# Kernel tuning notes

Hardware: AMD Instinct MI355X
Metric: run time of the kernel (lower is better)

The kernel has to match this reference:

```python
import jax, jax.numpy as jnp
import numpy as np

N = 50000       # nodes
E = 800000      # edges (before self-loops)
F_IN = 128      # per-head input features (nfeat * t_size, t_size=1)
NHID = 128
NHEADS = 4
NCLASS = 64
NEG_SLOPE = 0.2   # GATConv leakyrelu negative_slope
ALPHA = 0.2       # outer LeakyReLU(alpha)


def setup_inputs():
    key = jax.random.key(0)
    ks = jax.random.split(key, 10)
    type_emb = jax.random.normal(ks[0], (NHEADS, N, F_IN), jnp.float32)
    edge = jax.random.randint(ks[1], (2, E), 0, N, dtype=jnp.int32)
    W = jax.random.normal(ks[2], (NHEADS, F_IN, NHID), jnp.float32) / np.sqrt(F_IN).astype(np.float32)
    att_src = jax.random.normal(ks[3], (NHEADS, NHID), jnp.float32) * 0.1
    att_dst = jax.random.normal(ks[4], (NHEADS, NHID), jnp.float32) * 0.1
    bias = jnp.zeros((NHEADS, NHID), jnp.float32)
    W_out = jax.random.normal(ks[5], (NHID * NHEADS, NCLASS), jnp.float32) / np.sqrt(NHID * NHEADS).astype(np.float32)
    att_src_out = jax.random.normal(ks[6], (NCLASS,), jnp.float32) * 0.1
    att_dst_out = jax.random.normal(ks[7], (NCLASS,), jnp.float32) * 0.1
    bias_out = jnp.zeros((NCLASS,), jnp.float32)
    return {"type_emb": type_emb, "edge": edge, "W": W, "att_src": att_src,
            "att_dst": att_dst, "bias": bias, "W_out": W_out,
            "att_src_out": att_src_out, "att_dst_out": att_dst_out,
            "bias_out": bias_out}


def _gat_conv(x, src, dst, W, a_src, a_dst, b):
    """PyG GATConv, heads=1, with self-loops already in (src, dst)."""
    xs = x @ W                                      # [N, H]
    e = jax.nn.leaky_relu((xs @ a_src)[src] + (xs @ a_dst)[dst], NEG_SLOPE)  # [E']
    # segment softmax over destination nodes (every node has a self-loop -> no empty segment)
    m = jax.ops.segment_max(e, dst, num_segments=N)
    ex = jnp.exp(e - m[dst])
    denom = jax.ops.segment_sum(ex, dst, num_segments=N)
    alpha = ex / denom[dst]                          # [E']
    out = jax.ops.segment_sum(alpha[:, None] * xs[src], dst, num_segments=N)  # [N, H]
    return out + b


def reference(type_emb, edge, W, att_src, att_dst, bias, W_out,
              att_src_out, att_dst_out, bias_out):
    loop = jnp.arange(N, dtype=edge.dtype)
    src = jnp.concatenate([edge[0], loop])
    dst = jnp.concatenate([edge[1], loop])
    # per-head GraphAttentionLayer: GATConv -> LeakyReLU(alpha) (dropout inactive)
    heads = [jax.nn.leaky_relu(
                 _gat_conv(type_emb[i], src, dst, W[i], att_src[i], att_dst[i], bias[i]),
                 ALPHA)
             for i in range(NHEADS)]
    x = jnp.concatenate(heads, axis=1)               # [N, NHID*NHEADS]
    y = jax.nn.leaky_relu(
            _gat_conv(x, src, dst, W_out, att_src_out, att_dst_out, bias_out),
            ALPHA)
    return jnp.tanh(y)                               # [N, NCLASS]
```

## Files before the change

kernel.cpp:

```cpp
#include <hip/hip_runtime.h>
#include <cmath>

#define NN 50000
#define EE 800000
#define ETOT (EE + NN)
#define NSCAN ((NN + 1023) / 1024)
#define SROWS 50048

typedef __bf16 v8bf __attribute__((ext_vector_type(8)));
typedef float f32x4 __attribute__((ext_vector_type(4)));

__device__ __forceinline__ float lrelu(float x){ return x > 0.0f ? x : 0.2f * x; }
__device__ __forceinline__ unsigned short f2bf_rne(float x){
  unsigned int u = __float_as_uint(x);
  u += 0x7fffu + ((u >> 16) & 1u);
  return (unsigned short)(u >> 16);
}
__device__ __forceinline__ float bf2f(unsigned short b){
  return __uint_as_float(((unsigned int)b) << 16);
}
__device__ __forceinline__ void fma8(float* acc, float w, uint4 u){
  acc[0] += w * __uint_as_float(u.x << 16);
  acc[1] += w * __uint_as_float(u.x & 0xffff0000u);
  acc[2] += w * __uint_as_float(u.y << 16);
  acc[3] += w * __uint_as_float(u.y & 0xffff0000u);
  acc[4] += w * __uint_as_float(u.z << 16);
  acc[5] += w * __uint_as_float(u.z & 0xffff0000u);
  acc[6] += w * __uint_as_float(u.w << 16);
  acc[7] += w * __uint_as_float(u.w & 0xffff0000u);
}

__global__ void k_hist(const int* __restrict__ dst, int* __restrict__ cnt){
  int i = blockIdx.x * 256 + threadIdx.x;
  if (i >= ETOT) return;
  int d = (i < EE) ? dst[i] : (i - EE);
  atomicAdd(&cnt[d], 1);
}

__global__ void k_scan1(const int* __restrict__ cnt, int* __restrict__ part){
  __shared__ int sm[256];
  int b = blockIdx.x, t = threadIdx.x;
  int base = b * 1024 + t * 4;
  int s = 0;
  #pragma unroll
  for (int j = 0; j < 4; j++) if (base + j < NN) s += cnt[base + j];
  sm[t] = s; __syncthreads();
  for (int off = 128; off; off >>= 1){
    if (t < off) sm[t] += sm[t + off];
    __syncthreads();
  }
  if (t == 0) part[b] = sm[0];
}

__global__ void k_scan2(const int* __restrict__ part, int* __restrict__ part2){
  if (threadIdx.x == 0 && blockIdx.x == 0){
    int run = 0;
    for (int i = 0; i < NSCAN; i++){ part2[i] = run; run += part[i]; }
  }
}

__global__ void k_scan3(const int* __restrict__ cnt, const int* __restrict__ part2,
                        int* __restrict__ rowptr){
  __shared__ int sm[256];
  int b = blockIdx.x, t = threadIdx.x;
  int base = b * 1024 + t * 4;
  int v[4]; int s = 0;
  #pragma unroll
  for (int j = 0; j < 4; j++){ v[j] = (base + j < NN) ? cnt[base + j] : 0; s += v[j]; }
  sm[t] = s; __syncthreads();
  for (int off = 1; off < 256; off <<= 1){
    int x = (t >= off) ? sm[t - off] : 0;
    __syncthreads();
    sm[t] += x;
    __syncthreads();
  }
  int run = part2[b] + sm[t] - s;
  #pragma unroll
  for (int j = 0; j < 4; j++){
    if (base + j < NN){ rowptr[base + j] = run; run += v[j]; }
  }
  if (b == 0 && t == 0) rowptr[NN] = ETOT;
}

__global__ void k_scatter(const int* __restrict__ src, const int* __restrict__ dst,
                          const int* __restrict__ rowptr, int* __restrict__ fill,
                          int* __restrict__ csr){
  int i = blockIdx.x * 256 + threadIdx.x;
  if (i >= ETOT) return;
  int s, d;
  if (i < EE){ s = src[i]; d = dst[i]; } else { s = d = i - EE; }
  int pos = rowptr[d] + atomicAdd(&fill[d], 1);
  csr[pos] = s;
}

__global__ void k_convB(const float* __restrict__ B, unsigned short* __restrict__ bh,
                        unsigned short* __restrict__ bl, int K, int N, int total){
  int i = blockIdx.x * 256 + threadIdx.x;
  if (i >= total) return;
  int per = K * N;
  int h = i / per, rem = i - h * per;
  int k = rem / N, n = rem - k * N;
  float x = B[i];
  unsigned short hb = f2bf_rne(x);
  unsigned short lb = f2bf_rne(x - bf2f(hb));
  size_t o = (size_t)h * per + ((size_t)(k >> 3) * N + n) * 8 + (k & 7);
  bh[o] = hb; bl[o] = lb;
}

template<int BN, int OSTR>
__global__ __launch_bounds__(256) void gemm_split(const float* __restrict__ A,
                                                  const unsigned short* __restrict__ Bh,
                                                  const unsigned short* __restrict__ Bl,
                                                  unsigned short* __restrict__ out,
                                                  int M, int K,
                                                  const float* __restrict__ att_s,
                                                  const float* __restrict__ att_d,
                                                  float* __restrict__ ssrc,
                                                  float* __restrict__ sdst){
  const int t = threadIdx.x;
  const int wv = t >> 6, lane = t & 63;
  const int m0 = blockIdx.x * 128;
  const int h = blockIdx.y;
  A  += (size_t)h * M * K;
  Bh += (size_t)h * (K >> 3) * BN * 8;
  Bl += (size_t)h * (K >> 3) * BN * 8;
  const int colOff = h * BN;

  __shared__ v8bf sAh[4][128];
  __shared__ v8bf sAl[4][128];
  __shared__ v8bf sBh[4][BN];
  __shared__ v8bf sBl[4][BN];

  f32x4 acc[2][BN / 16];
  #pragma unroll
  for (int i = 0; i < 2; i++)
    #pragma unroll
    for (int j = 0; j < BN / 16; j++){
      f32x4 z = {0.f, 0.f, 0.f, 0.f};
      acc[i][j] = z;
    }

  const int mRow = t & 127;
  const int kh = (t >> 7) * 16;
  const bool valid = (m0 + mRow) < M;
  const int q = lane >> 4, lm = lane & 15;

  for (int k0 = 0; k0 < K; k0 += 32){
    const float* ap = A + (size_t)(m0 + mRow) * K + k0 + kh;
    float4 v0, v1, v2, v3;
    if (valid){
      v0 = *(const float4*)(ap);
      v1 = *(const float4*)(ap + 4);
      v2 = *(const float4*)(ap + 8);
      v3 = *(const float4*)(ap + 12);
    } else {
      v0 = v1 = v2 = v3 = make_float4(0.f, 0.f, 0.f, 0.f);
    }
    #pragma unroll
    for (int g = 0; g < 2; g++){
      float xv[8];
      if (g == 0){ xv[0]=v0.x; xv[1]=v0.y; xv[2]=v0.z; xv[3]=v0.w; xv[4]=v1.x; xv[5]=v1.y; xv[6]=v1.z; xv[7]=v1.w; }
      else       { xv[0]=v2.x; xv[1]=v2.y; xv[2]=v2.z; xv[3]=v2.w; xv[4]=v3.x; xv[5]=v3.y; xv[6]=v3.z; xv[7]=v3.w; }
      union { v8bf v; unsigned short u[8]; } H, L;
      #pragma unroll
      for (int i = 0; i < 8; i++){
        unsigned short hb = f2bf_rne(xv[i]);
        H.u[i] = hb;
        L.u[i] = f2bf_rne(xv[i] - bf2f(hb));
      }
      int k8 = (kh >> 3) + g;
      sAh[k8][mRow] = H.v;
      sAl[k8][mRow] = L.v;
    }
    {
      const v8bf* gh = (const v8bf*)Bh + (size_t)(k0 >> 3) * BN;
      const v8bf* gl = (const v8bf*)Bl + (size_t)(k0 >> 3) * BN;
      v8bf* dh = &sBh[0][0];
      v8bf* dl = &sBl[0][0];
      #pragma unroll
      for (int i = t; i < 4 * BN; i += 256){ dh[i] = gh[i]; dl[i] = gl[i]; }
    }
    __syncthreads();
    v8bf ah[2], al[2];
    #pragma unroll
    for (int rt = 0; rt < 2; rt++){
      int m = wv * 32 + rt * 16 + lm;
      ah[rt] = sAh[q][m];
      al[rt] = sAl[q][m];
    }
    #pragma unroll
    for (int ct = 0; ct < BN / 16; ct++){
      v8bf bh = sBh[q][ct * 16 + lm];
      v8bf bl = sBl[q][ct * 16 + lm];
      #pragma unroll
      for (int rt = 0; rt < 2; rt++){
        acc[rt][ct] = __builtin_amdgcn_mfma_f32_16x16x32_bf16(ah[rt], bh, acc[rt][ct], 0, 0, 0);
        acc[rt][ct] = __builtin_amdgcn_mfma_f32_16x16x32_bf16(ah[rt], bl, acc[rt][ct], 0, 0, 0);
        acc[rt][ct] = __builtin_amdgcn_mfma_f32_16x16x32_bf16(al[rt], bh, acc[rt][ct], 0, 0, 0);
      }
    }
    __syncthreads();
  }

  float asv[BN / 16], adv[BN / 16];
  #pragma unroll
  for (int ct = 0; ct < BN / 16; ct++){
    asv[ct] = att_s[h * BN + ct * 16 + lm];
    adv[ct] = att_d[h * BN + ct * 16 + lm];
  }

  #pragma unroll
  for (int rt = 0; rt < 2; rt++){
    #pragma unroll
    for (int reg = 0; reg < 4; reg++){
      int r = m0 + wv * 32 + rt * 16 + q * 4 + reg;
      float d0 = 0.f, d1 = 0.f;
      #pragma unroll
      for (int ct = 0; ct < BN / 16; ct++){
        float v = acc[rt][ct][reg];
        d0 += v * asv[ct];
        d1 += v * adv[ct];
      }
      #pragma unroll
      for (int off = 1; off < 16; off <<= 1){
        d0 += __shfl_xor(d0, off, 64);
        d1 += __shfl_xor(d1, off, 64);
      }
      if (r < M){
        unsigned short* orow = out + (size_t)r * OSTR + colOff + lm;
        #pragma unroll
        for (int ct = 0; ct < BN / 16; ct++)
          orow[ct * 16] = f2bf_rne(acc[rt][ct][reg]);
        if (lm == 0){
          ssrc[(size_t)h * SROWS + r] = d0;
          sdst[(size_t)h * SROWS + r] = d1;
        }
      }
    }
  }
}

template<int BN, int OSTR>
__global__ __launch_bounds__(256) void gemm_ps(const unsigned short* __restrict__ Ah,
                                               const unsigned short* __restrict__ Al,
                                               const unsigned short* __restrict__ Bh,
                                               const unsigned short* __restrict__ Bl,
                                               unsigned short* __restrict__ out,
                                               int M, int K,
                                               const float* __restrict__ att_s,
                                               const float* __restrict__ att_d,
                                               float* __restrict__ ssrc,
                                               float* __restrict__ sdst){
  const int t = threadIdx.x;
  const int wv = t >> 6, lane = t & 63;
  const int m0 = blockIdx.x * 128;
  const int h = blockIdx.y;
  const int colOff = h * BN;

  __shared__ v8bf sAh[4][128];
  __shared__ v8bf sAl[4][128];
  __shared__ v8bf sBh[4][BN];
  __shared__ v8bf sBl[4][BN];

  f32x4 acc[2][BN / 16];
  #pragma unroll
  for (int i = 0; i < 2; i++)
    #pragma unroll
    for (int j = 0; j < BN / 16; j++){
      f32x4 z = {0.f, 0.f, 0.f, 0.f};
      acc[i][j] = z;
    }

  const int mRow = t & 127;
  const int kh = (t >> 7) * 16;
  const bool valid = (m0 + mRow) < M;
  const int q = lane >> 4, lm = lane & 15;

  for (int k0 = 0; k0 < K; k0 += 32){
    const unsigned short* aph = Ah + (size_t)(m0 + mRow) * K + k0 + kh;
    const unsigned short* apl = Al + (size_t)(m0 + mRow) * K + k0 + kh;
    uint4 h0, h1, l0, l1;
    if (valid){
      h0 = *(const uint4*)(aph);
      h1 = *(const uint4*)(aph + 8);
      l0 = *(const uint4*)(apl);
      l1 = *(const uint4*)(apl + 8);
    } else {
      h0 = h1 = l0 = l1 = make_uint4(0, 0, 0, 0);
    }
    int k8 = kh >> 3;
    sAh[k8][mRow]     = *(v8bf*)&h0;
    sAh[k8 + 1][mRow] = *(v8bf*)&h1;
    sAl[k8][mRow]     = *(v8bf*)&l0;
    sAl[k8 + 1][mRow] = *(v8bf*)&l1;
    {
      const v8bf* gh = (const v8bf*)Bh + (size_t)(k0 >> 3) * BN;
      const v8bf* gl = (const v8bf*)Bl + (size_t)(k0 >> 3) * BN;
      v8bf* dh = &sBh[0][0];
      v8bf* dl = &sBl[0][0];
      #pragma unroll
      for (int i = t; i < 4 * BN; i += 256){ dh[i] = gh[i]; dl[i] = gl[i]; }
    }
    __syncthreads();
    v8bf ah[2], al[2];
    #pragma unroll
    for (int rt = 0; rt < 2; rt++){
      int m = wv * 32 + rt * 16 + lm;
      ah[rt] = sAh[q][m];
      al[rt] = sAl[q][m];
    }
    #pragma unroll
    for (int ct = 0; ct < BN / 16; ct++){
      v8bf bh = sBh[q][ct * 16 + lm];
      v8bf bl = sBl[q][ct * 16 + lm];
      #pragma unroll
      for (int rt = 0; rt < 2; rt++){
        acc[rt][ct] = __builtin_amdgcn_mfma_f32_16x16x32_bf16(ah[rt], bh, acc[rt][ct], 0, 0, 0);
        acc[rt][ct] = __builtin_amdgcn_mfma_f32_16x16x32_bf16(ah[rt], bl, acc[rt][ct], 0, 0, 0);
        acc[rt][ct] = __builtin_amdgcn_mfma_f32_16x16x32_bf16(al[rt], bh, acc[rt][ct], 0, 0, 0);
      }
    }
    __syncthreads();
  }

  float asv[BN / 16], adv[BN / 16];
  #pragma unroll
  for (int ct = 0; ct < BN / 16; ct++){
    asv[ct] = att_s[h * BN + ct * 16 + lm];
    adv[ct] = att_d[h * BN + ct * 16 + lm];
  }

  #pragma unroll
  for (int rt = 0; rt < 2; rt++){
    #pragma unroll
    for (int reg = 0; reg < 4; reg++){
      int r = m0 + wv * 32 + rt * 16 + q * 4 + reg;
      float d0 = 0.f, d1 = 0.f;
      #pragma unroll
      for (int ct = 0; ct < BN / 16; ct++){
        float v = acc[rt][ct][reg];
        d0 += v * asv[ct];
        d1 += v * adv[ct];
      }
      #pragma unroll
      for (int off = 1; off < 16; off <<= 1){
        d0 += __shfl_xor(d0, off, 64);
        d1 += __shfl_xor(d1, off, 64);
      }
      if (r < M){
        unsigned short* orow = out + (size_t)r * OSTR + colOff + lm;
        #pragma unroll
        for (int ct = 0; ct < BN / 16; ct++)
          orow[ct * 16] = f2bf_rne(acc[rt][ct][reg]);
        if (lm == 0){
          ssrc[(size_t)h * SROWS + r] = d0;
          sdst[(size_t)h * SROWS + r] = d1;
        }
      }
    }
  }
}

__global__ __launch_bounds__(256) void k_agg1(const int* __restrict__ rowptr,
                                              const int* __restrict__ csr,
                                              const float* __restrict__ ssrc,
                                              const float* __restrict__ sdst,
                                              const unsigned short* __restrict__ xs_all,
                                              const float* __restrict__ bias,
                                              unsigned short* __restrict__ x1h,
                                              unsigned short* __restrict__ x1l){
  int tid = blockIdx.x * 256 + threadIdx.x;
  int n = tid >> 4;
  int lm = threadIdx.x & 15;
  int h = blockIdx.y;
  if (n >= NN) return;
  int start = rowptr[n], end = rowptr[n + 1];
  const float* sp = ssrc + (size_t)h * SROWS;
  float sdn = sdst[(size_t)h * SROWS + n];
  const uint4* xp = (const uint4*)xs_all + h * 16 + lm;

  float sloc = 0.f;
  float acc[8];
  #pragma unroll
  for (int i = 0; i < 8; i++) acc[i] = 0.f;

  int e = start;
  int sA = csr[e];
  float svA = sp[sA];
  uint4 uA = xp[(size_t)sA * 64];
  for (; e + 1 < end; e++){
    int sB = csr[e + 1];
    float svB = sp[sB];
    uint4 uB = xp[(size_t)sB * 64];
    float w = __expf(lrelu(svA + sdn));
    sloc += w;
    fma8(acc, w, uA);
    svA = svB; uA = uB;
  }
  float w = __expf(lrelu(svA + sdn));
  sloc += w;
  fma8(acc, w, uA);

  float inv = 1.f / sloc;

  const float* bp = bias + h * 128 + lm * 8;
  float4 b0 = *(const float4*)bp, b1 = *(const float4*)(bp + 4);
  float bb[8] = {b0.x, b0.y, b0.z, b0.w, b1.x, b1.y, b1.z, b1.w};
  union { uint4 q; unsigned short u[8]; } HH, LL;
  #pragma unroll
  for (int i = 0; i < 8; i++){
    float o = lrelu(acc[i] * inv + bb[i]);
    unsigned short hb = f2bf_rne(o);
    HH.u[i] = hb;
    LL.u[i] = f2bf_rne(o - bf2f(hb));
  }
  size_t ofs = (size_t)n * 512 + h * 128 + lm * 8;
  *(uint4*)(x1h + ofs) = HH.q;
  *(uint4*)(x1l + ofs) = LL.q;
}

__global__ __launch_bounds__(256) void k_agg2(const int* __restrict__ rowptr,
                                              const int* __restrict__ csr,
                                              const float* __restrict__ ssrc,
                                              const float* __restrict__ sdst,
                                              const unsigned short* __restrict__ xs2,
                                              const float* __restrict__ bias,
                                              float* __restrict__ outp){
  int tid = blockIdx.x * 256 + threadIdx.x;
  int n = tid >> 3;
  int lm = threadIdx.x & 7;
  if (n >= NN) return;
  int start = rowptr[n], end = rowptr[n + 1];
  float sdn = sdst[n];
  const uint4* xp = (const uint4*)xs2 + lm;

  float sloc = 0.f;
  float acc[8];
  #pragma unroll
  for (int i = 0; i < 8; i++) acc[i] = 0.f;

  int e = start;
  int sA = csr[e];
  float svA = ssrc[sA];
  uint4 uA = xp[(size_t)sA * 8];
  for (; e + 1 < end; e++){
    int sB = csr[e + 1];
    float svB = ssrc[sB];
    uint4 uB = xp[(size_t)sB * 8];
    float w = __expf(lrelu(svA + sdn));
    sloc += w;
    fma8(acc, w, uA);
    svA = svB; uA = uB;
  }
  float w = __expf(lrelu(svA + sdn));
  sloc += w;
  fma8(acc, w, uA);

  float inv = 1.f / sloc;

  float o[8];
  #pragma unroll
  for (int i = 0; i < 8; i++)
    o[i] = tanhf(lrelu(acc[i] * inv + bias[lm * 8 + i]));
  float* op = outp + (size_t)n * 64 + lm * 8;
  *(float4*)op       = make_float4(o[0], o[1], o[2], o[3]);
  *(float4*)(op + 4) = make_float4(o[4], o[5], o[6], o[7]);
}

extern "C" void kernel_launch(void* const* d_in, const int* in_sizes, int n_in,
                              void* d_out, int out_size, void* d_ws, size_t ws_size,
                              hipStream_t stream){
  const float* type_emb  = (const float*)d_in[0];
  const int*   edge      = (const int*)d_in[1];
  const float* W         = (const float*)d_in[2];
  const float* att_src   = (const float*)d_in[3];
  const float* att_dst   = (const float*)d_in[4];
  const float* bias      = (const float*)d_in[5];
  const float* W_out     = (const float*)d_in[6];
  const float* att_src_o = (const float*)d_in[7];
  const float* att_dst_o = (const float*)d_in[8];
  const float* bias_o    = (const float*)d_in[9];
  float* out = (float*)d_out;
  (void)in_sizes; (void)n_in; (void)out_size; (void)ws_size;

  char* ws = (char*)d_ws;
  size_t off = 0;
  auto alloc = [&](size_t bytes) -> void* {
    void* p = ws + off;
    off = (off + bytes + 255) & ~(size_t)255;
    return p;
  };
  unsigned short* xs_all = (unsigned short*)alloc((size_t)NN * 512 * 2);
  unsigned short* x1h    = (unsigned short*)alloc((size_t)NN * 512 * 2);
  unsigned short* x1l    = (unsigned short*)alloc((size_t)NN * 512 * 2);
  unsigned short* xs2    = (unsigned short*)alloc((size_t)NN * 64 * 2);
  float* ssrc1 = (float*)alloc((size_t)4 * SROWS * 4);
  float* sdst1 = (float*)alloc((size_t)4 * SROWS * 4);
  float* ssrc2 = (float*)alloc((size_t)SROWS * 4);
  float* sdst2 = (float*)alloc((size_t)SROWS * 4);
  int* cnt    = (int*)alloc((size_t)NN * 4);
  int* rowptr = (int*)alloc((size_t)(NN + 1) * 4);
  int* fill   = (int*)alloc((size_t)NN * 4);
  int* csr    = (int*)alloc((size_t)ETOT * 4);
  int* p1     = (int*)alloc((size_t)NSCAN * 4 + 256);
  int* p2     = (int*)alloc((size_t)NSCAN * 4 + 256);
  unsigned short* Bh1 = (unsigned short*)alloc((size_t)4 * 128 * 128 * 2);
  unsigned short* Bl1 = (unsigned short*)alloc((size_t)4 * 128 * 128 * 2);
  unsigned short* Bh2 = (unsigned short*)alloc((size_t)512 * 64 * 2);
  unsigned short* Bl2 = (unsigned short*)alloc((size_t)512 * 64 * 2);

  hipMemsetAsync(cnt, 0, (size_t)NN * 4, stream);
  hipMemsetAsync(fill, 0, (size_t)NN * 4, stream);
  k_hist<<<(ETOT + 255) / 256, 256, 0, stream>>>(edge + EE, cnt);
  k_scan1<<<NSCAN, 256, 0, stream>>>(cnt, p1);
  k_scan2<<<1, 64, 0, stream>>>(p1, p2);
  k_scan3<<<NSCAN, 256, 0, stream>>>(cnt, p2, rowptr);
  k_scatter<<<(ETOT + 255) / 256, 256, 0, stream>>>(edge, edge + EE, rowptr, fill, csr);

  k_convB<<<(4 * 128 * 128 + 255) / 256, 256, 0, stream>>>(W, Bh1, Bl1, 128, 128, 4 * 128 * 128);
  k_convB<<<(512 * 64 + 255) / 256, 256, 0, stream>>>(W_out, Bh2, Bl2, 512, 64, 512 * 64);

  gemm_split<128, 512><<<dim3(391, 4), 256, 0, stream>>>(
      type_emb, Bh1, Bl1, xs_all, NN, 128, att_src, att_dst, ssrc1, sdst1);
  k_agg1<<<dim3(3125, 4), 256, 0, stream>>>(rowptr, csr, ssrc1, sdst1, xs_all, bias, x1h, x1l);

  gemm_ps<64, 64><<<dim3(391, 1), 256, 0, stream>>>(
      x1h, x1l, Bh2, Bl2, xs2, NN, 512, att_src_o, att_dst_o, ssrc2, sdst2);
  k_agg2<<<1563, 256, 0, stream>>>(rowptr, csr, ssrc2, sdst2, xs2, bias_o, out);
}
```

Measured before the change: 461.2 us.

## Sort nodes by degree, deepen gather prefetch, use packed FMA in aggregation

Adds a degree-bucketing pass (histogram, scan, scatter) that yields a node order grouped by in-degree. Both aggregation kernels process nodes in that order so wavefront lanes handle similar-length neighbour lists, which reduces divergence and idle lanes. The gather loop is also deepened to prefetch two edges ahead, and accumulation uses 2-wide float vectors to encourage packed FMA. In exchange there are three extra small kernels with atomics, and output writes plus row gathers become less sequential because node order is permuted.

After: 756.2 us. +64.0%, slower.

```diff
diff --git a/kernel.cpp b/kernel.cpp
--- a/kernel.cpp
+++ b/kernel.cpp
@@ -9,6 +9,7 @@
 
 typedef __bf16 v8bf __attribute__((ext_vector_type(8)));
 typedef float f32x4 __attribute__((ext_vector_type(4)));
+typedef float f32x2 __attribute__((ext_vector_type(2)));
 
 __device__ __forceinline__ float lrelu(float x){ return x > 0.0f ? x : 0.2f * x; }
 __device__ __forceinline__ unsigned short f2bf_rne(float x){
@@ -19,15 +20,17 @@
 __device__ __forceinline__ float bf2f(unsigned short b){
   return __uint_as_float(((unsigned int)b) << 16);
 }
-__device__ __forceinline__ void fma8(float* acc, float w, uint4 u){
-  acc[0] += w * __uint_as_float(u.x << 16);
-  acc[1] += w * __uint_as_float(u.x & 0xffff0000u);
-  acc[2] += w * __uint_as_float(u.y << 16);
-  acc[3] += w * __uint_as_float(u.y & 0xffff0000u);
-  acc[4] += w * __uint_as_float(u.z << 16);
-  acc[5] += w * __uint_as_float(u.z & 0xffff0000u);
-  acc[6] += w * __uint_as_float(u.w << 16);
-  acc[7] += w * __uint_as_float(u.w & 0xffff0000u);
+__device__ __forceinline__ void fma8p(f32x2* acc, float w, uint4 u){
+  f32x2 w2 = {w, w};
+  f32x2 a0, a1, a2, a3;
+  a0[0] = __uint_as_float(u.x << 16); a0[1] = __uint_as_float(u.x & 0xffff0000u);
+  a1[0] = __uint_as_float(u.y << 16); a1[1] = __uint_as_float(u.y & 0xffff0000u);
+  a2[0] = __uint_as_float(u.z << 16); a2[1] = __uint_as_float(u.z & 0xffff0000u);
+  a3[0] = __uint_as_float(u.w << 16); a3[1] = __uint_as_float(u.w & 0xffff0000u);
+  acc[0] += w2 * a0;
+  acc[1] += w2 * a1;
+  acc[2] += w2 * a2;
+  acc[3] += w2 * a3;
 }
 
 __global__ void k_hist(const int* __restrict__ dst, int* __restrict__ cnt){
@@ -91,6 +94,28 @@
   if (i < EE){ s = src[i]; d = dst[i]; } else { s = d = i - EE; }
   int pos = rowptr[d] + atomicAdd(&fill[d], 1);
   csr[pos] = s;
+}
+
+__global__ void k_dhist(const int* __restrict__ cnt, int* __restrict__ bcnt){
+  int n = blockIdx.x * 256 + threadIdx.x;
+  if (n >= NN) return;
+  atomicAdd(&bcnt[min(cnt[n], 63)], 1);
+}
+
+__global__ void k_dscan(const int* __restrict__ bcnt, int* __restrict__ boff){
+  if (threadIdx.x == 0 && blockIdx.x == 0){
+    int run = 0;
+    for (int i = 0; i < 64; i++){ boff[i] = run; run += bcnt[i]; }
+  }
+}
+
+__global__ void k_dscatter(const int* __restrict__ cnt, const int* __restrict__ boff,
+                           int* __restrict__ bfill, int* __restrict__ nodeorder){
+  int n = blockIdx.x * 256 + threadIdx.x;
+  if (n >= NN) return;
+  int b = min(cnt[n], 63);
+  int pos = boff[b] + atomicAdd(&bfill[b], 1);
+  nodeorder[pos] = n;
 }
 
 __global__ void k_convB(const float* __restrict__ B, unsigned short* __restrict__ bh,
@@ -363,6 +388,7 @@
 
 __global__ __launch_bounds__(256) void k_agg1(const int* __restrict__ rowptr,
                                               const int* __restrict__ csr,
+                                              const int* __restrict__ nodeorder,
                                               const float* __restrict__ ssrc,
                                               const float* __restrict__ sdst,
                                               const unsigned short* __restrict__ xs_all,
@@ -370,36 +396,51 @@
                                               unsigned short* __restrict__ x1h,
                                               unsigned short* __restrict__ x1l){
   int tid = blockIdx.x * 256 + threadIdx.x;
-  int n = tid >> 4;
+  int idx = tid >> 4;
   int lm = threadIdx.x & 15;
   int h = blockIdx.y;
-  if (n >= NN) return;
+  if (idx >= NN) return;
+  int n = nodeorder[idx];
   int start = rowptr[n], end = rowptr[n + 1];
   const float* sp = ssrc + (size_t)h * SROWS;
   float sdn = sdst[(size_t)h * SROWS + n];
   const uint4* xp = (const uint4*)xs_all + h * 16 + lm;
 
   float sloc = 0.f;
-  float acc[8];
-  #pragma unroll
-  for (int i = 0; i < 8; i++) acc[i] = 0.f;
+  f32x2 acc[4];
+  #pragma unroll
+  for (int i = 0; i < 4; i++){ f32x2 z = {0.f, 0.f}; acc[i] = z; }
 
   int e = start;
   int sA = csr[e];
   float svA = sp[sA];
   uint4 uA = xp[(size_t)sA * 64];
-  for (; e + 1 < end; e++){
+  bool hasB = (e + 1 < end);
+  float svB = 0.f;
+  uint4 uB = make_uint4(0, 0, 0, 0);
+  if (hasB){
     int sB = csr[e + 1];
-    float svB = sp[sB];
-    uint4 uB = xp[(size_t)sB * 64];
+    svB = sp[sB];
+    uB = xp[(size_t)sB * 64];
+  }
+  for (; e + 2 < end; e++){
+    int sC = csr[e + 2];
+    float svC = sp[sC];
+    uint4 uC = xp[(size_t)sC * 64];
     float w = __expf(lrelu(svA + sdn));
     sloc += w;
-    fma8(acc, w, uA);
+    fma8p(acc, w, uA);
     svA = svB; uA = uB;
+    svB = svC; uB = uC;
   }
   float w = __expf(lrelu(svA + sdn));
   sloc += w;
-  fma8(acc, w, uA);
+  fma8p(acc, w, uA);
+  if (hasB){
+    w = __expf(lrelu(svB + sdn));
+    sloc += w;
+    fma8p(acc, w, uB);
+  }
 
   float inv = 1.f / sloc;
 
@@ -409,7 +450,7 @@
   union { uint4 q; unsigned short u[8]; } HH, LL;
   #pragma unroll
   for (int i = 0; i < 8; i++){
-    float o = lrelu(acc[i] * inv + bb[i]);
+    float o = lrelu(acc[i >> 1][i & 1] * inv + bb[i]);
     unsigned short hb = f2bf_rne(o);
     HH.u[i] = hb;
     LL.u[i] = f2bf_rne(o - bf2f(hb));
@@ -421,47 +462,63 @@
 
 __global__ __launch_bounds__(256) void k_agg2(const int* __restrict__ rowptr,
                                               const int* __restrict__ csr,
+                                              const int* __restrict__ nodeorder,
                                               const float* __restrict__ ssrc,
                                               const float* __restrict__ sdst,
                                               const unsigned short* __restrict__ xs2,
                                               const float* __restrict__ bias,
                                               float* __restrict__ outp){
   int tid = blockIdx.x * 256 + threadIdx.x;
-  int n = tid >> 3;
+  int idx = tid >> 3;
   int lm = threadIdx.x & 7;
-  if (n >= NN) return;
+  if (idx >= NN) return;
+  int n = nodeorder[idx];
   int start = rowptr[n], end = rowptr[n + 1];
   float sdn = sdst[n];
   const uint4* xp = (const uint4*)xs2 + lm;
 
   float sloc = 0.f;
-  float acc[8];
-  #pragma unroll
-  for (int i = 0; i < 8; i++) acc[i] = 0.f;
+  f32x2 acc[4];
+  #pragma unroll
+  for (int i = 0; i < 4; i++){ f32x2 z = {0.f, 0.f}; acc[i] = z; }
 
   int e = start;
   int sA = csr[e];
   float svA = ssrc[sA];
   uint4 uA = xp[(size_t)sA * 8];
-  for (; e + 1 < end; e++){
+  bool hasB = (e + 1 < end);
+  float svB = 0.f;
+  uint4 uB = make_uint4(0, 0, 0, 0);
+  if (hasB){
     int sB = csr[e + 1];
-    float svB = ssrc[sB];
-    uint4 uB = xp[(size_t)sB * 8];
+    svB = ssrc[sB];
+    uB = xp[(size_t)sB * 8];
+  }
+  for (; e + 2 < end; e++){
+    int sC = csr[e + 2];
+    float svC = ssrc[sC];
+    uint4 uC = xp[(size_t)sC * 8];
     float w = __expf(lrelu(svA + sdn));
     sloc += w;
-    fma8(acc, w, uA);
+    fma8p(acc, w, uA);
     svA = svB; uA = uB;
+    svB = svC; uB = uC;
   }
   float w = __expf(lrelu(svA + sdn));
   sloc += w;
-  fma8(acc, w, uA);
+  fma8p(acc, w, uA);
+  if (hasB){
+    w = __expf(lrelu(svB + sdn));
+    sloc += w;
+    fma8p(acc, w, uB);
+  }
 
   float inv = 1.f / sloc;
 
   float o[8];
   #pragma unroll
   for (int i = 0; i < 8; i++)
-    o[i] = tanhf(lrelu(acc[i] * inv + bias[lm * 8 + i]));
+    o[i] = tanhf(lrelu(acc[i >> 1][i & 1] * inv + bias[lm * 8 + i]));
   float* op = outp + (size_t)n * 64 + lm * 8;
   *(float4*)op       = make_float4(o[0], o[1], o[2], o[3]);
   *(float4*)(op + 4) = make_float4(o[4], o[5], o[6], o[7]);
@@ -504,6 +561,10 @@
   int* csr    = (int*)alloc((size_t)ETOT * 4);
   int* p1     = (int*)alloc((size_t)NSCAN * 4 + 256);
   int* p2     = (int*)alloc((size_t)NSCAN * 4 + 256);
+  int* bcnt   = (int*)alloc(64 * 4);
+  int* boff   = (int*)alloc(64 * 4);
+  int* bfill  = (int*)alloc(64 * 4);
+  int* nodeorder = (int*)alloc((size_t)NN * 4);
   unsigned short* Bh1 = (unsigned short*)alloc((size_t)4 * 128 * 128 * 2);
   unsigned short* Bl1 = (unsigned short*)alloc((size_t)4 * 128 * 128 * 2);
   unsigned short* Bh2 = (unsigned short*)alloc((size_t)512 * 64 * 2);
@@ -511,20 +572,25 @@
 
   hipMemsetAsync(cnt, 0, (size_t)NN * 4, stream);
   hipMemsetAsync(fill, 0, (size_t)NN * 4, stream);
+  hipMemsetAsync(bcnt, 0, 64 * 4, stream);
+  hipMemsetAsync(bfill, 0, 64 * 4, stream);
   k_hist<<<(ETOT + 255) / 256, 256, 0, stream>>>(edge + EE, cnt);
   k_scan1<<<NSCAN, 256, 0, stream>>>(cnt, p1);
   k_scan2<<<1, 64, 0, stream>>>(p1, p2);
   k_scan3<<<NSCAN, 256, 0, stream>>>(cnt, p2, rowptr);
   k_scatter<<<(ETOT + 255) / 256, 256, 0, stream>>>(edge, edge + EE, rowptr, fill, csr);
+  k_dhist<<<(NN + 255) / 256, 256, 0, stream>>>(cnt, bcnt);
+  k_dscan<<<1, 64, 0, stream>>>(bcnt, boff);
+  k_dscatter<<<(NN + 255) / 256, 256, 0, stream>>>(cnt, boff, bfill, nodeorder);
 
   k_convB<<<(4 * 128 * 128 + 255) / 256, 256, 0, stream>>>(W, Bh1, Bl1, 128, 128, 4 * 128 * 128);
   k_convB<<<(512 * 64 + 255) / 256, 256, 0, stream>>>(W_out, Bh2, Bl2, 512, 64, 512 * 64);
 
   gemm_split<128, 512><<<dim3(391, 4), 256, 0, stream>>>(
       type_emb, Bh1, Bl1, xs_all, NN, 128, att_src, att_dst, ssrc1, sdst1);
-  k_agg1<<<dim3(3125, 4), 256, 0, stream>>>(rowptr, csr, ssrc1, sdst1, xs_all, bias, x1h, x1l);
+  k_agg1<<<dim3(3125, 4), 256, 0, stream>>>(rowptr, csr, nodeorder, ssrc1, sdst1, xs_all, bias, x1h, x1l);
 
   gemm_ps<64, 64><<<dim3(391, 1), 256, 0, stream>>>(
       x1h, x1l, Bh2, Bl2, xs2, NN, 512, att_src_o, att_dst_o, ssrc2, sdst2);
-  k_agg2<<<1563, 256, 0, stream>>>(rowptr, csr, ssrc2, sdst2, xs2, bias_o, out);
-}
+  k_agg2<<<1563, 256, 0, stream>>>(rowptr, csr, nodeorder, ssrc2, sdst2, xs2, bias_o, out);
+}
```
